# Kernel optimization log

Measured on AMD Instinct MI355X. Metric: run time of the kernel, lower is better.

Reference implementation:

```python
import jax, jax.numpy as jnp
import numpy as np

N = 4096
C = 128
L = 4
E = 131072
HEADS = 4
BN_EPS = 1e-5


def setup_inputs() -> dict:
    key = jax.random.key(0)
    ks = jax.random.split(key, 16)
    s = jnp.float32(0.05)

    def rn(k, shape):
        return jax.random.normal(k, shape, dtype=jnp.float32) * s

    return {
        "x": jax.random.normal(ks[0], (N, C), dtype=jnp.float32),
        "edge_index": jax.random.randint(ks[1], (2, E), 0, N, dtype=jnp.int64) if jax.config.read("jax_enable_x64") else jax.random.randint(ks[1], (2, E), 0, N, dtype=jnp.int32),
        "gin_w1": rn(ks[2], (L, C, C)), "gin_b1": jnp.zeros((L, C), jnp.float32),
        "gin_w2": rn(ks[3], (L, C, C)), "gin_b2": jnp.zeros((L, C), jnp.float32),
        "attn_in_w": rn(ks[4], (L, 3 * C, C)), "attn_in_b": jnp.zeros((L, 3 * C), jnp.float32),
        "attn_out_w": rn(ks[5], (L, C, C)), "attn_out_b": jnp.zeros((L, C), jnp.float32),
        "n1_g": jnp.ones((L, C), jnp.float32), "n1_b": jnp.zeros((L, C), jnp.float32),
        "n2_g": jnp.ones((L, C), jnp.float32), "n2_b": jnp.zeros((L, C), jnp.float32),
        "n3_g": jnp.ones((L, C), jnp.float32), "n3_b": jnp.zeros((L, C), jnp.float32),
        "mlp_w1": rn(ks[6], (L, 2 * C, C)), "mlp_b1": jnp.zeros((L, 2 * C), jnp.float32),
        "mlp_w2": rn(ks[7], (L, C, 2 * C)), "mlp_b2": jnp.zeros((L, C), jnp.float32),
        "head_w1": rn(ks[8], (C // 2, C)), "head_b1": jnp.zeros((C // 2,), jnp.float32),
        "head_w2": rn(ks[9], (C // 4, C // 2)), "head_b2": jnp.zeros((C // 4,), jnp.float32),
        "head_w3": rn(ks[10], (1, C // 4)), "head_b3": jnp.zeros((1,), jnp.float32),
    }


def _bn(x, g, b):
    # BatchNorm1d over the node dim, training-mode (biased var), eps=1e-5
    mu = x.mean(axis=0)
    var = x.var(axis=0)
    return g * (x - mu) * jax.lax.rsqrt(var + BN_EPS) + b


def _gin(x, src, dst, w1, b1, w2, b2):
    # GINConv with eps=0: nn(x + sum_{j in N(i)} x_j)
    agg = jax.ops.segment_sum(x[src], dst, num_segments=x.shape[0])
    h = x + agg
    h = jnp.maximum(h @ w1.T + b1, 0.0)
    return h @ w2.T + b2


def _mha(x, wi, bi, wo, bo):
    # torch.nn.MultiheadAttention self-attention over a single dense batch of N nodes
    n, c = x.shape
    d = c // HEADS
    q, k, v = jnp.split(x @ wi.T + bi, 3, axis=-1)
    q = q.reshape(n, HEADS, d)
    k = k.reshape(n, HEADS, d)
    v = v.reshape(n, HEADS, d)
    scores = jnp.einsum('nhd,mhd->hnm', q, k) / jnp.sqrt(jnp.asarray(d, x.dtype))
    a = jax.nn.softmax(scores, axis=-1)
    o = jnp.einsum('hnm,mhd->nhd', a, v).reshape(n, c)
    return o @ wo.T + bo


def _forward(x, edge_index, gin_w1, gin_b1, gin_w2, gin_b2, attn_in_w, attn_in_b,
             attn_out_w, attn_out_b, n1_g, n1_b, n2_g, n2_b, n3_g, n3_b,
             mlp_w1, mlp_b1, mlp_w2, mlp_b2, head_w1, head_b1, head_w2, head_b2,
             head_w3, head_b3):
    src, dst = edge_index[0], edge_index[1]
    for i in range(L):
        # local GIN branch + residual + batch norm
        h1 = _bn(_gin(x, src, dst, gin_w1[i], gin_b1[i], gin_w2[i], gin_b2[i]) + x, n1_g[i], n1_b[i])
        # global attention branch + residual + batch norm
        h2 = _bn(_mha(x, attn_in_w[i], attn_in_b[i], attn_out_w[i], attn_out_b[i]) + x, n2_g[i], n2_b[i])
        h = h1 + h2
        # GPSConv MLP (C -> 2C -> C) with residual and final batch norm
        m = jnp.maximum(h @ mlp_w1[i].T + mlp_b1[i], 0.0) @ mlp_w2[i].T + mlp_b2[i]
        x = _bn(h + m, n3_g[i], n3_b[i])
    # head MLP: C -> C/2 -> C/4 -> 1
    h = jnp.maximum(x @ head_w1.T + head_b1, 0.0)
    h = jnp.maximum(h @ head_w2.T + head_b2, 0.0)
    return h @ head_w3.T + head_b3


def reference(x, edge_index, gin_w1, gin_b1, gin_w2, gin_b2, attn_in_w, attn_in_b,
              attn_out_w, attn_out_b, n1_g, n1_b, n2_g, n2_b, n3_g, n3_b,
              mlp_w1, mlp_b1, mlp_w2, mlp_b2, head_w1, head_b1, head_w2, head_b2,
              head_w3, head_b3):
    return _forward(x, edge_index, gin_w1, gin_b1, gin_w2, gin_b2, attn_in_w, attn_in_b,
                    attn_out_w, attn_out_b, n1_g, n1_b, n2_g, n2_b, n3_g, n3_b,
                    mlp_w1, mlp_b1, mlp_w2, mlp_b2, head_w1, head_b1, head_w2, head_b2,
                    head_w3, head_b3)
```

## Files before the change

kernel.cpp:

```cpp
#include <hip/hip_runtime.h>

#define N_NODES 4096
#define C_DIM   128
#define L_LAYERS 4
#define E_EDGES 131072
#define H_HEADS 4
#define D_HEAD  32
#define NC      (N_NODES * C_DIM)
#define NCu     (N_NODES * C_DIM)
#define P_STRIDE 136
#define HS_STRIDE 152

typedef short bf16x8 __attribute__((ext_vector_type(8)));
typedef float f32x4  __attribute__((ext_vector_type(4)));

__device__ __forceinline__ unsigned short f2bf(float f) {
    unsigned int u = __float_as_uint(f);
    u += 0x7fffu + ((u >> 16) & 1u);
    return (unsigned short)(u >> 16);
}

__device__ __forceinline__ float bf_lo(unsigned int u) { return __uint_as_float(u << 16); }
__device__ __forceinline__ float bf_hi(unsigned int u) { return __uint_as_float(u & 0xffff0000u); }

__device__ __forceinline__ bf16x8 pack8(const float* v) {
    bf16x8 o;
#pragma unroll
    for (int i = 0; i < 8; ++i) o[i] = (short)f2bf(v[i]);
    return o;
}

__global__ __launch_bounds__(256) void hist_kernel(const int* __restrict__ ei,
                                                   int* __restrict__ deg) {
    int e = blockIdx.x * 256 + threadIdx.x;
    atomicAdd(&deg[ei[E_EDGES + e]], 1);
}

__global__ __launch_bounds__(256) void scan_kernel(const int* __restrict__ deg,
                                                   int* __restrict__ rowstart,
                                                   int* __restrict__ cursor) {
    __shared__ int ts[256];
    const int tid = threadIdx.x;
    int loc[16];
    int s = 0;
#pragma unroll
    for (int i = 0; i < 16; ++i) { loc[i] = s; s += deg[tid * 16 + i]; }
    ts[tid] = s;
    __syncthreads();
    for (int off = 1; off < 256; off <<= 1) {
        int t = (tid >= off) ? ts[tid - off] : 0;
        __syncthreads();
        if (tid >= off) ts[tid] += t;
        __syncthreads();
    }
    int off0 = ts[tid] - s;
#pragma unroll
    for (int i = 0; i < 16; ++i) {
        int v = off0 + loc[i];
        rowstart[tid * 16 + i] = v;
        cursor[tid * 16 + i] = v;
    }
    if (tid == 255) rowstart[4096] = off0 + s;
}

__global__ __launch_bounds__(256) void fill_kernel(const int* __restrict__ ei,
                                                   int* __restrict__ cursor,
                                                   int* __restrict__ csr_src) {
    int e = blockIdx.x * 256 + threadIdx.x;
    int d = ei[E_EDGES + e];
    int s = ei[e];
    int p = atomicAdd(&cursor[d], 1);
    csr_src[p] = s;
}

__global__ __launch_bounds__(256) void wcvt(const float* __restrict__ s0, const float* __restrict__ s1,
                                            const float* __restrict__ s2, const float* __restrict__ s3,
                                            const float* __restrict__ s4, const float* __restrict__ s5,
                                            unsigned short* __restrict__ wbf) {
    int i0 = (blockIdx.x * 256 + threadIdx.x) * 8;
    const float* src; int base;
    if      (i0 < 65536)  { src = s0; base = 0; }
    else if (i0 < 131072) { src = s1; base = 65536; }
    else if (i0 < 327680) { src = s2; base = 131072; }
    else if (i0 < 393216) { src = s3; base = 327680; }
    else if (i0 < 524288) { src = s4; base = 393216; }
    else                  { src = s5; base = 524288; }
    const float* p = src + (i0 - base);
    float t[8];
#pragma unroll
    for (int i = 0; i < 8; ++i) t[i] = p[i];
    *(bf16x8*)(wbf + i0) = pack8(t);
}

__global__ __launch_bounds__(256) void x2bf(const float* __restrict__ x,
                                            unsigned short* __restrict__ xb) {
    int i0 = (blockIdx.x * 256 + threadIdx.x) * 8;
    float t[8];
#pragma unroll
    for (int i = 0; i < 8; ++i) t[i] = x[i0 + i];
    *(bf16x8*)(xb + i0) = pack8(t);
}

__global__ __launch_bounds__(256, 8) void qkv_gather(const unsigned short* __restrict__ xb,
                                                     const unsigned short* __restrict__ Wbf,
                                                     const float* __restrict__ bias,
                                                     unsigned short* __restrict__ Qb,
                                                     unsigned short* __restrict__ Kb,
                                                     unsigned short* __restrict__ VT,
                                                     const int* __restrict__ rowstart,
                                                     const int* __restrict__ csr_src,
                                                     unsigned int* __restrict__ hsum,
                                                     float* __restrict__ ssz) {
    const int b = blockIdx.x;
    const int tid = threadIdx.x;
    if (b < 1536) {
        const int ct = b % 6, rt = b / 6;
        const int wv = tid >> 6;
        const int lane = tid & 63, lg = lane >> 4, ll = lane & 15;
        const int rowbase = rt * 16;
        const int colbase = ct * 64 + wv * 16;

        const unsigned short* Ap = xb  + (size_t)(rowbase + ll) * 128 + lg * 8;
        const unsigned short* Wp = Wbf + (size_t)(colbase + ll) * 128 + lg * 8;

        f32x4 acc = {0.f, 0.f, 0.f, 0.f};
#pragma unroll
        for (int k = 0; k < 128; k += 32) {
            bf16x8 a = *(const bf16x8*)(Ap + k);
            bf16x8 w = *(const bf16x8*)(Wp + k);
            acc = __builtin_amdgcn_mfma_f32_16x16x32_bf16(a, w, acc, 0, 0, 0);
        }

        const float qsc = 0.25506973f;
        const int col = colbase + ll;
        const float bi = bias[col];
#pragma unroll
        for (int r = 0; r < 4; ++r) {
            const int row = rowbase + lg * 4 + r;
            float v = acc[r] + bi;
            if (col < 128) {
                int hh = col >> 5, d = col & 31;
                Qb[((size_t)hh * N_NODES + row) * D_HEAD + d] = f2bf(v * qsc);
            } else if (col < 256) {
                int c2 = col - 128, hh = c2 >> 5, d = c2 & 31;
                Kb[((size_t)hh * N_NODES + row) * D_HEAD + d] = f2bf(v);
            } else {
                int c2 = col - 256, hh = c2 >> 5, d = c2 & 31;
                VT[((size_t)hh * D_HEAD + d) * N_NODES + row] = f2bf(v);
            }
        }
    } else {
        if (b == 1536) {
            ssz[tid] = 0.f; ssz[256 + tid] = 0.f; ssz[512 + tid] = 0.f;
        }
        const int node = (b - 1536) * 4 + (tid >> 6);
        const int lane = tid & 63;
        const unsigned int* xu = (const unsigned int*)xb;
        const int beg = rowstart[node], end = rowstart[node + 1];
        unsigned int su = xu[(size_t)node * 64 + lane];
        float ax = bf_lo(su), ay = bf_hi(su);
        float bx = 0.f, by = 0.f;
        int e = beg;
        for (; e + 4 <= end; e += 4) {
            int s0 = csr_src[e], s1 = csr_src[e + 1], s2 = csr_src[e + 2], s3 = csr_src[e + 3];
            unsigned int u0 = xu[(size_t)s0 * 64 + lane];
            unsigned int u1 = xu[(size_t)s1 * 64 + lane];
            unsigned int u2 = xu[(size_t)s2 * 64 + lane];
            unsigned int u3 = xu[(size_t)s3 * 64 + lane];
            ax += bf_lo(u0) + bf_lo(u1); ay += bf_hi(u0) + bf_hi(u1);
            bx += bf_lo(u2) + bf_lo(u3); by += bf_hi(u2) + bf_hi(u3);
        }
        for (; e < end; ++e) {
            unsigned int u0 = xu[(size_t)csr_src[e] * 64 + lane];
            ax += bf_lo(u0); ay += bf_hi(u0);
        }
        float ox = ax + bx, oy = ay + by;
        hsum[(size_t)node * 64 + lane] = (unsigned int)f2bf(ox) | ((unsigned int)f2bf(oy) << 16);
    }
}

__global__ __launch_bounds__(512, 4) void attn_gin1(const unsigned short* __restrict__ Qb,
                                                    const unsigned short* __restrict__ Kb,
                                                    const unsigned short* __restrict__ VT,
                                                    unsigned short* __restrict__ ob,
                                                    const unsigned short* __restrict__ hsum,
                                                    const unsigned short* __restrict__ W1,
                                                    const float* __restrict__ bias1,
                                                    unsigned short* __restrict__ t1out) {
    __shared__ __align__(16) unsigned short Pl[8 * 32 * P_STRIDE];
    float (*Ouns)[32][33] = (float (*)[32][33])(void*)Pl;
    float (*Llp)[32] = (float (*)[32])(void*)(Pl + 8 * 32 * 33 * 2);

    const int b   = blockIdx.x;
    const int tid = threadIdx.x;
    const int wv  = tid >> 6;
    const int lane = tid & 63;
    const int lg  = lane >> 4;
    const int ll  = lane & 15;

    if (b >= 512) {
        const int rowbase = (b - 512) * 16;
        const int colbase = wv * 16;
        const unsigned short* Ap = hsum + (size_t)(rowbase + ll) * 128 + lg * 8;
        const unsigned short* Wp = W1 + (size_t)(colbase + ll) * 128 + lg * 8;
        f32x4 acc = {0.f, 0.f, 0.f, 0.f};
#pragma unroll
        for (int k = 0; k < 128; k += 32) {
            bf16x8 a = *(const bf16x8*)(Ap + k);
            bf16x8 w = *(const bf16x8*)(Wp + k);
            acc = __builtin_amdgcn_mfma_f32_16x16x32_bf16(a, w, acc, 0, 0, 0);
        }
        const int col = colbase + ll;
        const float bi = bias1[col];
#pragma unroll
        for (int r = 0; r < 4; ++r) {
            const int row = rowbase + lg * 4 + r;
            float v = fmaxf(acc[r] + bi, 0.f);
            t1out[(size_t)row * 128 + col] = f2bf(v);
        }
        return;
    }

    const int h   = b >> 7;
    const int q0  = (b & 127) * 32;

    const unsigned short* Qh = Qb + ((size_t)h * N_NODES + q0) * D_HEAD;
    const unsigned short* Kh = Kb + (size_t)h * N_NODES * D_HEAD;
    const unsigned short* Vh = VT + (size_t)h * D_HEAD * N_NODES;

    bf16x8 qf0 = *(const bf16x8*)(Qh + ll * D_HEAD + lg * 8);
    bf16x8 qf1 = *(const bf16x8*)(Qh + (16 + ll) * D_HEAD + lg * 8);

    f32x4 oacc00 = {0.f,0.f,0.f,0.f}, oacc01 = {0.f,0.f,0.f,0.f};
    f32x4 oacc10 = {0.f,0.f,0.f,0.f}, oacc11 = {0.f,0.f,0.f,0.f};
    float l0[4] = {0.f,0.f,0.f,0.f}, l1[4] = {0.f,0.f,0.f,0.f};

    unsigned short* Pw = Pl + wv * (32 * P_STRIDE);
    const int k0 = wv * (N_NODES / 8);

    for (int t = 0; t < (N_NODES / 8) / 128; ++t) {
        const int kt = k0 + t * 128;

        float s0[8][4], s1[8][4];
#pragma unroll
        for (int kc = 0; kc < 8; ++kc) {
            bf16x8 kf = *(const bf16x8*)(Kh + (size_t)(kt + kc * 16 + ll) * D_HEAD + lg * 8);
            f32x4 z = {0.f, 0.f, 0.f, 0.f};
            f32x4 d0 = __builtin_amdgcn_mfma_f32_16x16x32_bf16(qf0, kf, z, 0, 0, 0);
            f32x4 d1 = __builtin_amdgcn_mfma_f32_16x16x32_bf16(qf1, kf, z, 0, 0, 0);
#pragma unroll
            for (int r = 0; r < 4; ++r) { s0[kc][r] = d0[r]; s1[kc][r] = d1[r]; }
        }

#pragma unroll
        for (int r = 0; r < 4; ++r) {
            float a = 0.f, bb = 0.f;
#pragma unroll
            for (int kc = 0; kc < 8; ++kc) {
                float p0 = exp2f(s0[kc][r]); s0[kc][r] = p0; a += p0;
                float p1 = exp2f(s1[kc][r]); s1[kc][r] = p1; bb += p1;
            }
#pragma unroll
            for (int off = 1; off < 16; off <<= 1) {
                a += __shfl_xor(a, off, 64);
                bb += __shfl_xor(bb, off, 64);
            }
            l0[r] += a;
            l1[r] += bb;
        }

#pragma unroll
        for (int kc = 0; kc < 8; ++kc)
#pragma unroll
            for (int r = 0; r < 4; ++r) {
                Pw[(lg * 4 + r) * P_STRIDE + kc * 16 + ll]      = f2bf(s0[kc][r]);
                Pw[(16 + lg * 4 + r) * P_STRIDE + kc * 16 + ll] = f2bf(s1[kc][r]);
            }
        asm volatile("" ::: "memory");

#pragma unroll
        for (int kc2 = 0; kc2 < 4; ++kc2) {
            bf16x8 va = *(const bf16x8*)(Vh + (size_t)ll * N_NODES + kt + kc2 * 32 + lg * 8);
            bf16x8 vb = *(const bf16x8*)(Vh + (size_t)(16 + ll) * N_NODES + kt + kc2 * 32 + lg * 8);
            bf16x8 pf0 = *(const bf16x8*)(Pw + ll * P_STRIDE + kc2 * 32 + lg * 8);
            bf16x8 pf1 = *(const bf16x8*)(Pw + (16 + ll) * P_STRIDE + kc2 * 32 + lg * 8);
            oacc00 = __builtin_amdgcn_mfma_f32_16x16x32_bf16(pf0, va, oacc00, 0, 0, 0);
            oacc01 = __builtin_amdgcn_mfma_f32_16x16x32_bf16(pf0, vb, oacc01, 0, 0, 0);
            oacc10 = __builtin_amdgcn_mfma_f32_16x16x32_bf16(pf1, va, oacc10, 0, 0, 0);
            oacc11 = __builtin_amdgcn_mfma_f32_16x16x32_bf16(pf1, vb, oacc11, 0, 0, 0);
        }
    }

    __syncthreads();

#pragma unroll
    for (int r = 0; r < 4; ++r) {
        Ouns[wv][lg * 4 + r][ll]           = oacc00[r];
        Ouns[wv][lg * 4 + r][16 + ll]      = oacc01[r];
        Ouns[wv][16 + lg * 4 + r][ll]      = oacc10[r];
        Ouns[wv][16 + lg * 4 + r][16 + ll] = oacc11[r];
    }
    if (ll == 0) {
#pragma unroll
        for (int r = 0; r < 4; ++r) {
            Llp[wv][lg * 4 + r]      = l0[r];
            Llp[wv][16 + lg * 4 + r] = l1[r];
        }
    }
    __syncthreads();

    {
        const int row = tid >> 4, col = tid & 15;
        float L = 0.f, oa = 0.f, obv = 0.f;
#pragma unroll
        for (int w = 0; w < 8; ++w) {
            L   += Llp[w][row];
            oa  += Ouns[w][row][col];
            obv += Ouns[w][row][16 + col];
        }
        float inv = 1.f / L;
        ob[(size_t)(q0 + row) * C_DIM + h * D_HEAD + col]      = f2bf(oa * inv);
        ob[(size_t)(q0 + row) * C_DIM + h * D_HEAD + 16 + col] = f2bf(obv * inv);
    }
}

template <int K>
__global__ __launch_bounds__(256, 8) void gemm_bf(const unsigned short* __restrict__ Abf,
                                                  const unsigned short* __restrict__ Wbf,
                                                  const float* __restrict__ bias,
                                                  const float* __restrict__ resid,
                                                  float* __restrict__ outf,
                                                  unsigned short* __restrict__ outb,
                                                  float* __restrict__ stats,
                                                  const int J, const int relu) {
    const int tid = threadIdx.x;
    const int wv = tid >> 6;
    const int lane = tid & 63, lg = lane >> 4, ll = lane & 15;
    const int rowbase = blockIdx.y * 16;
    const int colbase = blockIdx.x * 64 + wv * 16;

    const unsigned short* Ap = Abf + (size_t)(rowbase + ll) * K + lg * 8;
    const unsigned short* Wp = Wbf + (size_t)(colbase + ll) * K + lg * 8;

    f32x4 acc = {0.f, 0.f, 0.f, 0.f};
#pragma unroll
    for (int k = 0; k < K; k += 32) {
        bf16x8 a = *(const bf16x8*)(Ap + k);
        bf16x8 b = *(const bf16x8*)(Wp + k);
        acc = __builtin_amdgcn_mfma_f32_16x16x32_bf16(a, b, acc, 0, 0, 0);
    }

    const int col = colbase + ll;
    const float bi = bias[col];
    float sv = 0.f, sv2 = 0.f;
#pragma unroll
    for (int r = 0; r < 4; ++r) {
        const int row = rowbase + lg * 4 + r;
        float v = acc[r] + bi;
        if (resid) v += resid[(size_t)row * J + col];
        if (relu) v = fmaxf(v, 0.f);
        if (outf) outf[(size_t)row * J + col] = v;
        if (outb) outb[(size_t)row * J + col] = f2bf(v);
        sv += v; sv2 += v * v;
    }
    if (stats) {
        sv  += __shfl_xor(sv, 16, 64);  sv  += __shfl_xor(sv, 32, 64);
        sv2 += __shfl_xor(sv2, 16, 64); sv2 += __shfl_xor(sv2, 32, 64);
        if (lg == 0) {
            atomicAdd(&stats[col], sv);
            atomicAdd(&stats[C_DIM + col], sv2);
        }
    }
}

__global__ __launch_bounds__(256, 8) void gemm2x(const unsigned short* __restrict__ A0,
                                                 const unsigned short* __restrict__ W0,
                                                 const float* __restrict__ bias0,
                                                 float* __restrict__ out0,
                                                 float* __restrict__ stats0,
                                                 const unsigned short* __restrict__ A1,
                                                 const unsigned short* __restrict__ W1,
                                                 const float* __restrict__ bias1,
                                                 float* __restrict__ out1,
                                                 float* __restrict__ stats1,
                                                 const float* __restrict__ resid) {
    const int b = blockIdx.x;
    const int which = b >> 9;
    const int bl = b & 511;
    const unsigned short* Abf = which ? A1 : A0;
    const unsigned short* Wbf = which ? W1 : W0;
    const float* bias = which ? bias1 : bias0;
    float* outf  = which ? out1 : out0;
    float* stats = which ? stats1 : stats0;

    const int tid = threadIdx.x;
    const int wv = tid >> 6;
    const int lane = tid & 63, lg = lane >> 4, ll = lane & 15;
    const int rowbase = (bl >> 1) * 16;
    const int colbase = (bl & 1) * 64 + wv * 16;

    const unsigned short* Ap = Abf + (size_t)(rowbase + ll) * 128 + lg * 8;
    const unsigned short* Wp = Wbf + (size_t)(colbase + ll) * 128 + lg * 8;

    f32x4 acc = {0.f, 0.f, 0.f, 0.f};
#pragma unroll
    for (int k = 0; k < 128; k += 32) {
        bf16x8 a = *(const bf16x8*)(Ap + k);
        bf16x8 w = *(const bf16x8*)(Wp + k);
        acc = __builtin_amdgcn_mfma_f32_16x16x32_bf16(a, w, acc, 0, 0, 0);
    }

    const int col = colbase + ll;
    const float bi = bias[col];
    float sv = 0.f, sv2 = 0.f;
#pragma unroll
    for (int r = 0; r < 4; ++r) {
        const int row = rowbase + lg * 4 + r;
        float v = acc[r] + bi + resid[(size_t)row * 128 + col];
        outf[(size_t)row * 128 + col] = v;
        sv += v; sv2 += v * v;
    }
    sv  += __shfl_xor(sv, 16, 64);  sv  += __shfl_xor(sv, 32, 64);
    sv2 += __shfl_xor(sv2, 16, 64); sv2 += __shfl_xor(sv2, 32, 64);
    if (lg == 0) {
        atomicAdd(&stats[col], sv);
        atomicAdd(&stats[128 + col], sv2);
    }
}

__global__ __launch_bounds__(256, 8) void mlp1_fused(const float* __restrict__ g1p,
                                                     const float* __restrict__ a2p,
                                                     const float* __restrict__ st1,
                                                     const float* __restrict__ st2,
                                                     const float* __restrict__ g1v,
                                                     const float* __restrict__ b1v,
                                                     const float* __restrict__ g2v,
                                                     const float* __restrict__ b2v,
                                                     const unsigned short* __restrict__ Wbf,
                                                     const float* __restrict__ bias,
                                                     float* __restrict__ hbuf,
                                                     unsigned short* __restrict__ t2out) {
    __shared__ __align__(16) unsigned short hs[16 * HS_STRIDE];
    __shared__ float scl[4][128];

    const int tid = threadIdx.x;
    const int bx = blockIdx.x;
    const int rowbase = blockIdx.y * 16;
    const float inv_n = 1.f / N_NODES;

    if (tid < 128) {
        const int ch = tid;
        float m1 = st1[ch] * inv_n;
        float v1 = st1[128 + ch] * inv_n - m1 * m1;
        float r1 = rsqrtf(v1 + 1e-5f);
        float sc1 = g1v[ch] * r1;
        scl[0][ch] = sc1;
        scl[1][ch] = b1v[ch] - m1 * sc1;
        float m2 = st2[ch] * inv_n;
        float v2 = st2[128 + ch] * inv_n - m2 * m2;
        float r2 = rsqrtf(v2 + 1e-5f);
        float sc2 = g2v[ch] * r2;
        scl[2][ch] = sc2;
        scl[3][ch] = b2v[ch] - m2 * sc2;
    }
    __syncthreads();

#pragma unroll
    for (int j = tid; j < 512; j += 256) {
        const int r = j >> 5, cq = (j & 31) * 4;
        float4 v1 = *(const float4*)(g1p + (size_t)(rowbase + r) * 128 + cq);
        float4 v2 = *(const float4*)(a2p + (size_t)(rowbase + r) * 128 + cq);
        float h0 = v1.x * scl[0][cq]     + scl[1][cq]     + v2.x * scl[2][cq]     + scl[3][cq];
        float h1 = v1.y * scl[0][cq + 1] + scl[1][cq + 1] + v2.y * scl[2][cq + 1] + scl[3][cq + 1];
        float h2 = v1.z * scl[0][cq + 2] + scl[1][cq + 2] + v2.z * scl[2][cq + 2] + scl[3][cq + 2];
        float h3 = v1.w * scl[0][cq + 3] + scl[1][cq + 3] + v2.w * scl[2][cq + 3] + scl[3][cq + 3];
        ushort4 u;
        u.x = f2bf(h0); u.y = f2bf(h1); u.z = f2bf(h2); u.w = f2bf(h3);
        *(ushort4*)(&hs[r * HS_STRIDE + cq]) = u;
        if (bx == 0) {
            float4 o = {h0, h1, h2, h3};
            *(float4*)(hbuf + (size_t)(rowbase + r) * 128 + cq) = o;
        }
    }
    __syncthreads();

    const int wv = tid >> 6;
    const int lane = tid & 63, lg = lane >> 4, ll = lane & 15;
    const int colbase = bx * 64 + wv * 16;
    const unsigned short* Wp = Wbf + (size_t)(colbase + ll) * 128 + lg * 8;

    f32x4 acc = {0.f, 0.f, 0.f, 0.f};
#pragma unroll
    for (int k = 0; k < 128; k += 32) {
        bf16x8 a = *(const bf16x8*)(&hs[ll * HS_STRIDE + k + lg * 8]);
        bf16x8 w = *(const bf16x8*)(Wp + k);
        acc = __builtin_amdgcn_mfma_f32_16x16x32_bf16(a, w, acc, 0, 0, 0);
    }

    const int col = colbase + ll;
    const float bi = bias[col];
#pragma unroll
    for (int r = 0; r < 4; ++r) {
        const int row = rowbase + lg * 4 + r;
        float v = fmaxf(acc[r] + bi, 0.f);
        t2out[(size_t)row * 256 + col] = f2bf(v);
    }
}

__global__ __launch_bounds__(256) void bn_apply(const float* __restrict__ p,
                                                const float* __restrict__ st,
                                                const float* __restrict__ gv,
                                                const float* __restrict__ bv,
                                                float* __restrict__ out,
                                                unsigned short* __restrict__ outb) {
    int idx = blockIdx.x * 256 + threadIdx.x;
    int c4 = (idx & 31) * 4;
    const float inv_n = 1.f / N_NODES;
    float sc[4], sh[4];
#pragma unroll
    for (int c = 0; c < 4; ++c) {
        int ch = c4 + c;
        float m = st[ch] * inv_n;
        float vv = st[C_DIM + ch] * inv_n - m * m;
        float r = rsqrtf(vv + 1e-5f);
        sc[c] = gv[ch] * r; sh[c] = bv[ch] - m * sc[c];
    }
    float4 v = ((const float4*)p)[idx];
    float4 o;
    o.x = v.x * sc[0] + sh[0];
    o.y = v.y * sc[1] + sh[1];
    o.z = v.z * sc[2] + sh[2];
    o.w = v.w * sc[3] + sh[3];
    ((float4*)out)[idx] = o;
    ushort4 ub;
    ub.x = f2bf(o.x); ub.y = f2bf(o.y); ub.z = f2bf(o.z); ub.w = f2bf(o.w);
    *(ushort4*)(outb + (size_t)idx * 4) = ub;
}

__global__ __launch_bounds__(256) void head_fused(const float* __restrict__ x,
                                                  const float* __restrict__ w1,
                                                  const float* __restrict__ b1,
                                                  const float* __restrict__ w2,
                                                  const float* __restrict__ b2,
                                                  const float* __restrict__ w3,
                                                  const float* __restrict__ b3,
                                                  float* __restrict__ out) {
    __shared__ __align__(16) float xs[8][128];
    __shared__ __align__(16) float hs2[8][64];
    const int tid = threadIdx.x;
    const int n = tid >> 5;
    const int g = tid & 31;
    const int node0 = blockIdx.x * 8;

    {
        int r = tid >> 5, q = tid & 31;
        *(float4*)(&xs[r][q * 4]) = *(const float4*)(x + (size_t)(node0 + r) * 128 + q * 4);
    }
    __syncthreads();

    {
        float acc0 = b1[g], acc1 = b1[g + 32];
        const float* wa = w1 + (size_t)g * 128;
        const float* wb = w1 + (size_t)(g + 32) * 128;
#pragma unroll 8
        for (int k = 0; k < 128; k += 4) {
            float4 xv = *(const float4*)(&xs[n][k]);
            float4 va = *(const float4*)(wa + k);
            float4 vb = *(const float4*)(wb + k);
            acc0 += xv.x * va.x + xv.y * va.y + xv.z * va.z + xv.w * va.w;
            acc1 += xv.x * vb.x + xv.y * vb.y + xv.z * vb.z + xv.w * vb.w;
        }
        hs2[n][g]      = fmaxf(acc0, 0.f);
        hs2[n][g + 32] = fmaxf(acc1, 0.f);
    }
    __syncthreads();

    {
        float acc = b2[g];
        const float* wr = w2 + (size_t)g * 64;
#pragma unroll 8
        for (int k = 0; k < 64; k += 4) {
            float4 hv = *(const float4*)(&hs2[n][k]);
            float4 wv = *(const float4*)(wr + k);
            acc += hv.x * wv.x + hv.y * wv.y + hv.z * wv.z + hv.w * wv.w;
        }
        float t = fmaxf(acc, 0.f) * w3[g];
#pragma unroll
        for (int off = 1; off < 32; off <<= 1) t += __shfl_xor(t, off, 64);
        if (g == 0) out[node0 + n] = t + b3[0];
    }
}

extern "C" void kernel_launch(void* const* d_in, const int* in_sizes, int n_in,
                              void* d_out, int out_size, void* d_ws, size_t ws_size,
                              hipStream_t stream) {
    (void)in_sizes; (void)n_in; (void)out_size; (void)ws_size;
    const float* x_in   = (const float*)d_in[0];
    const int*   ei     = (const int*)d_in[1];
    const float* gin_w1 = (const float*)d_in[2];
    const float* gin_b1 = (const float*)d_in[3];
    const float* gin_w2 = (const float*)d_in[4];
    const float* gin_b2 = (const float*)d_in[5];
    const float* ain_w  = (const float*)d_in[6];
    const float* ain_b  = (const float*)d_in[7];
    const float* aout_w = (const float*)d_in[8];
    const float* aout_b = (const float*)d_in[9];
    const float* n1_g   = (const float*)d_in[10];
    const float* n1_b   = (const float*)d_in[11];
    const float* n2_g   = (const float*)d_in[12];
    const float* n2_b   = (const float*)d_in[13];
    const float* n3_g   = (const float*)d_in[14];
    const float* n3_b   = (const float*)d_in[15];
    const float* mlp_w1 = (const float*)d_in[16];
    const float* mlp_b1 = (const float*)d_in[17];
    const float* mlp_w2 = (const float*)d_in[18];
    const float* mlp_b2 = (const float*)d_in[19];
    const float* h_w1   = (const float*)d_in[20];
    const float* h_b1   = (const float*)d_in[21];
    const float* h_w2   = (const float*)d_in[22];
    const float* h_b2   = (const float*)d_in[23];
    const float* h_w3   = (const float*)d_in[24];
    const float* h_b3   = (const float*)d_in[25];

    float* f = (float*)d_ws;
    float* g1   = f;
    float* m3   = f;
    float* a2   = f + 1 * (size_t)NC;
    float* hbuf = f + 2 * (size_t)NC;
    float* xA   = f + 3 * (size_t)NC;
    float* xB   = f + 4 * (size_t)NC;
    unsigned short* R1  = (unsigned short*)(f + 5 * (size_t)NC);
    unsigned short* Qb      = R1;
    unsigned short* Kb      = R1 + (size_t)NCu;
    unsigned short* VT      = R1 + 2 * (size_t)NCu;
    unsigned short* t2_bf   = R1;
    unsigned short* R2      = R1 + 3 * (size_t)NCu;
    unsigned short* ao_bf   = R2;
    unsigned short* hsum_bf = (unsigned short*)a2;
    unsigned short* t1_bf   = (unsigned short*)hbuf;
    unsigned short* xbf     = R2 + (size_t)NCu;
    unsigned short* wbf     = xbf + (size_t)NCu;
    float* ss    = (float*)(wbf + 655360);
    int* ibase    = (int*)(ss + 768);
    int* deg      = ibase;
    int* rowstart = ibase + 4096;
    int* cursor   = ibase + 4096 + 4098;
    int* csr_src  = ibase + 4096 + 4098 + 4096;

    const int OG1 = 0, OG2 = 65536, OAI = 131072, OAO = 327680, OM1 = 393216, OM2 = 524288;

    hipMemsetAsync(deg, 0, 4096 * sizeof(int), stream);
    hist_kernel<<<E_EDGES / 256, 256, 0, stream>>>(ei, deg);
    scan_kernel<<<1, 256, 0, stream>>>(deg, rowstart, cursor);
    fill_kernel<<<E_EDGES / 256, 256, 0, stream>>>(ei, cursor, csr_src);
    wcvt<<<320, 256, 0, stream>>>(gin_w1, gin_w2, ain_w, aout_w, mlp_w1, mlp_w2, wbf);
    x2bf<<<NC / 2048, 256, 0, stream>>>(x_in, xbf);

    for (int i = 0; i < L_LAYERS; ++i) {
        const float* xin = (i == 0) ? x_in : ((i & 1) ? xA : xB);
        float* xout = (i & 1) ? xB : xA;
        const float* gb1 = gin_b1 + (size_t)i * C_DIM;
        const float* gb2 = gin_b2 + (size_t)i * C_DIM;
        const float* aib = ain_b + (size_t)i * 3 * C_DIM;
        const float* aob = aout_b + (size_t)i * C_DIM;
        const float* mb1 = mlp_b1 + (size_t)i * 2 * C_DIM;
        const float* mb2 = mlp_b2 + (size_t)i * C_DIM;

        qkv_gather<<<2560, 256, 0, stream>>>(xbf, wbf + OAI + (size_t)i * 49152, aib,
                                             Qb, Kb, VT, rowstart, csr_src,
                                             (unsigned int*)hsum_bf, ss);
        attn_gin1<<<768, 512, 0, stream>>>(Qb, Kb, VT, ao_bf,
                                           hsum_bf, wbf + OG1 + (size_t)i * 16384, gb1, t1_bf);
        gemm2x<<<1024, 256, 0, stream>>>(t1_bf, wbf + OG2 + (size_t)i * 16384, gb2, g1, ss,
                                         ao_bf, wbf + OAO + (size_t)i * 16384, aob, a2, ss + 256,
                                         xin);
        mlp1_fused<<<dim3(4, 256), 256, 0, stream>>>(g1, a2, ss, ss + 256,
                                                     n1_g + (size_t)i * C_DIM, n1_b + (size_t)i * C_DIM,
                                                     n2_g + (size_t)i * C_DIM, n2_b + (size_t)i * C_DIM,
                                                     wbf + OM1 + (size_t)i * 32768, mb1,
                                                     hbuf, t2_bf);
        gemm_bf<256><<<dim3(2, 256), 256, 0, stream>>>(t2_bf, wbf + OM2 + (size_t)i * 32768,
                                                       mb2, hbuf, m3, nullptr, ss + 512, 128, 0);
        bn_apply<<<512, 256, 0, stream>>>(m3, ss + 512,
                                          n3_g + (size_t)i * C_DIM, n3_b + (size_t)i * C_DIM,
                                          xout, xbf);
    }

    const float* xf = xB;
    head_fused<<<N_NODES / 8, 256, 0, stream>>>(xf, h_w1, h_b1, h_w2, h_b2, h_w3, h_b3,
                                                (float*)d_out);
}
```

Measured before the change: 403.6 us.

## Fuse both MLP GEMMs into one kernel keeping hidden activations in LDS

Merges the MLP first layer (with BN1/BN2 combine) and the second-layer GEMM into a single kernel per 16-row tile. The 2C hidden activation and the residual h stay in shared memory instead of going through global memory, which removes one kernel launch and the t2/hbuf round trips. In exchange the grid shrinks from 1024+512 blocks to 256 blocks, each doing more serial work, and uses more LDS, so occupancy and parallelism drop.

Result: faster. 383.5 us (-5.0%).

```diff
diff --git a/kernel.cpp b/kernel.cpp
--- a/kernel.cpp
+++ b/kernel.cpp
@@ -10,6 +10,7 @@
 #define NCu     (N_NODES * C_DIM)
 #define P_STRIDE 136
 #define HS_STRIDE 152
+#define T2S       264
 
 typedef short bf16x8 __attribute__((ext_vector_type(8)));
 typedef float f32x4  __attribute__((ext_vector_type(4)));
@@ -321,55 +322,6 @@
         float inv = 1.f / L;
         ob[(size_t)(q0 + row) * C_DIM + h * D_HEAD + col]      = f2bf(oa * inv);
         ob[(size_t)(q0 + row) * C_DIM + h * D_HEAD + 16 + col] = f2bf(obv * inv);
-    }
-}
-
-template <int K>
-__global__ __launch_bounds__(256, 8) void gemm_bf(const unsigned short* __restrict__ Abf,
-                                                  const unsigned short* __restrict__ Wbf,
-                                                  const float* __restrict__ bias,
-                                                  const float* __restrict__ resid,
-                                                  float* __restrict__ outf,
-                                                  unsigned short* __restrict__ outb,
-                                                  float* __restrict__ stats,
-                                                  const int J, const int relu) {
-    const int tid = threadIdx.x;
-    const int wv = tid >> 6;
-    const int lane = tid & 63, lg = lane >> 4, ll = lane & 15;
-    const int rowbase = blockIdx.y * 16;
-    const int colbase = blockIdx.x * 64 + wv * 16;
-
-    const unsigned short* Ap = Abf + (size_t)(rowbase + ll) * K + lg * 8;
-    const unsigned short* Wp = Wbf + (size_t)(colbase + ll) * K + lg * 8;
-
-    f32x4 acc = {0.f, 0.f, 0.f, 0.f};
-#pragma unroll
-    for (int k = 0; k < K; k += 32) {
-        bf16x8 a = *(const bf16x8*)(Ap + k);
-        bf16x8 b = *(const bf16x8*)(Wp + k);
-        acc = __builtin_amdgcn_mfma_f32_16x16x32_bf16(a, b, acc, 0, 0, 0);
-    }
-
-    const int col = colbase + ll;
-    const float bi = bias[col];
-    float sv = 0.f, sv2 = 0.f;
-#pragma unroll
-    for (int r = 0; r < 4; ++r) {
-        const int row = rowbase + lg * 4 + r;
-        float v = acc[r] + bi;
-        if (resid) v += resid[(size_t)row * J + col];
-        if (relu) v = fmaxf(v, 0.f);
-        if (outf) outf[(size_t)row * J + col] = v;
-        if (outb) outb[(size_t)row * J + col] = f2bf(v);
-        sv += v; sv2 += v * v;
-    }
-    if (stats) {
-        sv  += __shfl_xor(sv, 16, 64);  sv  += __shfl_xor(sv, 32, 64);
-        sv2 += __shfl_xor(sv2, 16, 64); sv2 += __shfl_xor(sv2, 32, 64);
-        if (lg == 0) {
-            atomicAdd(&stats[col], sv);
-            atomicAdd(&stats[C_DIM + col], sv2);
-        }
     }
 }
 
@@ -428,24 +380,27 @@
     }
 }
 
-__global__ __launch_bounds__(256, 8) void mlp1_fused(const float* __restrict__ g1p,
-                                                     const float* __restrict__ a2p,
-                                                     const float* __restrict__ st1,
-                                                     const float* __restrict__ st2,
-                                                     const float* __restrict__ g1v,
-                                                     const float* __restrict__ b1v,
-                                                     const float* __restrict__ g2v,
-                                                     const float* __restrict__ b2v,
-                                                     const unsigned short* __restrict__ Wbf,
-                                                     const float* __restrict__ bias,
-                                                     float* __restrict__ hbuf,
-                                                     unsigned short* __restrict__ t2out) {
+__global__ __launch_bounds__(256) void mlp_fused(const float* __restrict__ g1p,
+                                                 const float* __restrict__ a2p,
+                                                 const float* __restrict__ st1,
+                                                 const float* __restrict__ st2,
+                                                 const float* __restrict__ g1v,
+                                                 const float* __restrict__ b1v,
+                                                 const float* __restrict__ g2v,
+                                                 const float* __restrict__ b2v,
+                                                 const unsigned short* __restrict__ W1bf,
+                                                 const float* __restrict__ bias1,
+                                                 const unsigned short* __restrict__ W2bf,
+                                                 const float* __restrict__ bias2,
+                                                 float* __restrict__ m3out,
+                                                 float* __restrict__ stats3) {
+    __shared__ float hf[16][132];
     __shared__ __align__(16) unsigned short hs[16 * HS_STRIDE];
+    __shared__ __align__(16) unsigned short t2s[16 * T2S];
     __shared__ float scl[4][128];
 
     const int tid = threadIdx.x;
-    const int bx = blockIdx.x;
-    const int rowbase = blockIdx.y * 16;
+    const int rowbase = blockIdx.x * 16;
     const float inv_n = 1.f / N_NODES;
 
     if (tid < 128) {
@@ -474,36 +429,64 @@
         float h1 = v1.y * scl[0][cq + 1] + scl[1][cq + 1] + v2.y * scl[2][cq + 1] + scl[3][cq + 1];
         float h2 = v1.z * scl[0][cq + 2] + scl[1][cq + 2] + v2.z * scl[2][cq + 2] + scl[3][cq + 2];
         float h3 = v1.w * scl[0][cq + 3] + scl[1][cq + 3] + v2.w * scl[2][cq + 3] + scl[3][cq + 3];
+        hf[r][cq] = h0; hf[r][cq + 1] = h1; hf[r][cq + 2] = h2; hf[r][cq + 3] = h3;
         ushort4 u;
         u.x = f2bf(h0); u.y = f2bf(h1); u.z = f2bf(h2); u.w = f2bf(h3);
         *(ushort4*)(&hs[r * HS_STRIDE + cq]) = u;
-        if (bx == 0) {
-            float4 o = {h0, h1, h2, h3};
-            *(float4*)(hbuf + (size_t)(rowbase + r) * 128 + cq) = o;
-        }
     }
     __syncthreads();
 
     const int wv = tid >> 6;
     const int lane = tid & 63, lg = lane >> 4, ll = lane & 15;
-    const int colbase = bx * 64 + wv * 16;
-    const unsigned short* Wp = Wbf + (size_t)(colbase + ll) * 128 + lg * 8;
-
-    f32x4 acc = {0.f, 0.f, 0.f, 0.f};
-#pragma unroll
-    for (int k = 0; k < 128; k += 32) {
-        bf16x8 a = *(const bf16x8*)(&hs[ll * HS_STRIDE + k + lg * 8]);
-        bf16x8 w = *(const bf16x8*)(Wp + k);
-        acc = __builtin_amdgcn_mfma_f32_16x16x32_bf16(a, w, acc, 0, 0, 0);
-    }
-
-    const int col = colbase + ll;
-    const float bi = bias[col];
-#pragma unroll
-    for (int r = 0; r < 4; ++r) {
-        const int row = rowbase + lg * 4 + r;
-        float v = fmaxf(acc[r] + bi, 0.f);
-        t2out[(size_t)row * 256 + col] = f2bf(v);
+
+#pragma unroll
+    for (int ct = 0; ct < 4; ++ct) {
+        const int colbase = wv * 16 + ct * 64;
+        const unsigned short* Wp = W1bf + (size_t)(colbase + ll) * 128 + lg * 8;
+        f32x4 acc = {0.f, 0.f, 0.f, 0.f};
+#pragma unroll
+        for (int k = 0; k < 128; k += 32) {
+            bf16x8 a = *(const bf16x8*)(&hs[ll * HS_STRIDE + k + lg * 8]);
+            bf16x8 w = *(const bf16x8*)(Wp + k);
+            acc = __builtin_amdgcn_mfma_f32_16x16x32_bf16(a, w, acc, 0, 0, 0);
+        }
+        const int col = colbase + ll;
+        const float bi = bias1[col];
+#pragma unroll
+        for (int r = 0; r < 4; ++r) {
+            float v = fmaxf(acc[r] + bi, 0.f);
+            t2s[(lg * 4 + r) * T2S + col] = f2bf(v);
+        }
+    }
+    __syncthreads();
+
+#pragma unroll
+    for (int p = 0; p < 2; ++p) {
+        const int colbase = p * 64 + wv * 16;
+        const unsigned short* Wp = W2bf + (size_t)(colbase + ll) * 256 + lg * 8;
+        f32x4 acc = {0.f, 0.f, 0.f, 0.f};
+#pragma unroll
+        for (int k = 0; k < 256; k += 32) {
+            bf16x8 a = *(const bf16x8*)(&t2s[ll * T2S + k + lg * 8]);
+            bf16x8 w = *(const bf16x8*)(Wp + k);
+            acc = __builtin_amdgcn_mfma_f32_16x16x32_bf16(a, w, acc, 0, 0, 0);
+        }
+        const int col = colbase + ll;
+        const float bi = bias2[col];
+        float sv = 0.f, sv2 = 0.f;
+#pragma unroll
+        for (int r = 0; r < 4; ++r) {
+            const int row = lg * 4 + r;
+            float v = acc[r] + bi + hf[row][col];
+            m3out[(size_t)(rowbase + row) * 128 + col] = v;
+            sv += v; sv2 += v * v;
+        }
+        sv  += __shfl_xor(sv, 16, 64);  sv  += __shfl_xor(sv, 32, 64);
+        sv2 += __shfl_xor(sv2, 16, 64); sv2 += __shfl_xor(sv2, 32, 64);
+        if (lg == 0) {
+            atomicAdd(&stats3[col], sv);
+            atomicAdd(&stats3[128 + col], sv2);
+        }
     }
 }
 
@@ -633,7 +616,6 @@
     unsigned short* Qb      = R1;
     unsigned short* Kb      = R1 + (size_t)NCu;
     unsigned short* VT      = R1 + 2 * (size_t)NCu;
-    unsigned short* t2_bf   = R1;
     unsigned short* R2      = R1 + 3 * (size_t)NCu;
     unsigned short* ao_bf   = R2;
     unsigned short* hsum_bf = (unsigned short*)a2;
@@ -674,13 +656,12 @@
         gemm2x<<<1024, 256, 0, stream>>>(t1_bf, wbf + OG2 + (size_t)i * 16384, gb2, g1, ss,
                                          ao_bf, wbf + OAO + (size_t)i * 16384, aob, a2, ss + 256,
                                          xin);
-        mlp1_fused<<<dim3(4, 256), 256, 0, stream>>>(g1, a2, ss, ss + 256,
-                                                     n1_g + (size_t)i * C_DIM, n1_b + (size_t)i * C_DIM,
-                                                     n2_g + (size_t)i * C_DIM, n2_b + (size_t)i * C_DIM,
-                                                     wbf + OM1 + (size_t)i * 32768, mb1,
-                                                     hbuf, t2_bf);
-        gemm_bf<256><<<dim3(2, 256), 256, 0, stream>>>(t2_bf, wbf + OM2 + (size_t)i * 32768,
-                                                       mb2, hbuf, m3, nullptr, ss + 512, 128, 0);
+        mlp_fused<<<256, 256, 0, stream>>>(g1, a2, ss, ss + 256,
+                                           n1_g + (size_t)i * C_DIM, n1_b + (size_t)i * C_DIM,
+                                           n2_g + (size_t)i * C_DIM, n2_b + (size_t)i * C_DIM,
+                                           wbf + OM1 + (size_t)i * 32768, mb1,
+                                           wbf + OM2 + (size_t)i * 32768, mb2,
+                                           m3, ss + 512);
         bn_apply<<<512, 256, 0, stream>>>(m3, ss + 512,
                                           n3_g + (size_t)i * C_DIM, n3_b + (size_t)i * C_DIM,
                                           xout, xbf);
```
